# Optimization experiments

Measured on AMD Instinct MI355X. Metric: run time of the kernel, lower is better.

## Reference

```python
import jax, jax.numpy as jnp
import numpy as np

B, N, DEG, LOOKBACK, DIM, OUT = 256, 512, 16, 5, 64, 6
E = B * N * DEG            # 2,097,152 directed edges
NN = B * N                 # 131,072 nodes
K1 = int(np.ceil(0.8 * N))    # 410 nodes kept per graph after pool1
K2 = int(np.ceil(0.8 * K1))   # 328 nodes kept per graph after pool2


def setup_inputs():
    key = jax.random.key(0)
    ks = jax.random.split(key, 14)
    x = jax.random.normal(ks[0], (NN, LOOKBACK), jnp.float32)
    # per-graph random edges, then shift into the global node index space
    local = jax.random.randint(ks[1], (2, E), 0, N)
    offsets = jnp.repeat(jnp.arange(B, dtype=jnp.int32) * N, N * DEG)
    edge_index = local + offsets[None, :]

    def lin(k, fi, fo):
        return jax.random.normal(k, (fi, fo), jnp.float32) / np.sqrt(fi)

    return {
        "x": x,
        "edge_index": edge_index,
        "c1_Wl": lin(ks[2], LOOKBACK, DIM), "c1_bl": jnp.zeros((DIM,), jnp.float32),
        "c1_Wr": lin(ks[3], LOOKBACK, DIM),
        "pool1_w": jax.random.normal(ks[4], (DIM,), jnp.float32) / np.sqrt(DIM),
        "c2_Wl": lin(ks[5], DIM, DIM), "c2_bl": jnp.zeros((DIM,), jnp.float32),
        "c2_Wr": lin(ks[6], DIM, DIM),
        "pool2_w": jax.random.normal(ks[7], (DIM,), jnp.float32) / np.sqrt(DIM),
        "lin1_W": lin(ks[8], 2 * DIM, DIM), "lin1_b": jnp.zeros((DIM,), jnp.float32),
        "lin2_W": lin(ks[9], DIM, OUT), "lin2_b": jnp.zeros((OUT,), jnp.float32),
    }


def _sage(x, src, dst, valid, Wl, bl, Wr, n_nodes):
    # PyG SAGEConv: out = lin_l(mean_{j->i} x_j) + lin_r(x_i); empty nbhd -> 0
    msg = x[src] * valid[:, None]
    s = jax.ops.segment_sum(msg, dst, num_segments=n_nodes)
    deg = jax.ops.segment_sum(valid, dst, num_segments=n_nodes)
    mean = s / jnp.maximum(deg, 1.0)[:, None]
    return mean @ Wl + bl + x @ Wr


def _topk(x, w, nb, npg, k):
    # PyG TopKPooling: score = tanh(x.w/||w||), keep top-k per graph, scale kept rows
    score = jnp.tanh((x @ w) / jnp.linalg.norm(w))
    vals, idx = jax.lax.top_k(score.reshape(nb, npg), k)     # [nb, k]
    perm = (idx + (jnp.arange(nb) * npg)[:, None]).reshape(-1)
    return x[perm] * vals.reshape(-1, 1), perm


def _readout(x, nb, k):
    r = x.reshape(nb, k, -1)
    return jnp.concatenate([r.max(axis=1), r.mean(axis=1)], axis=1)  # [gmp | gap]


def reference(x, edge_index, c1_Wl, c1_bl, c1_Wr, pool1_w,
              c2_Wl, c2_bl, c2_Wr, pool2_w, lin1_W, lin1_b, lin2_W, lin2_b):
    src, dst = edge_index[0], edge_index[1]
    valid0 = jnp.ones((E,), jnp.float32)

    h = jax.nn.relu(_sage(x, src, dst, valid0, c1_Wl, c1_bl, c1_Wr, NN))
    h, perm1 = _topk(h, pool1_w, B, N, K1)
    x1 = _readout(h, B, K1)

    # filter_adj: remap edges to pooled node ids, mask dropped edges
    n1 = B * K1
    inv = jnp.full((NN,), -1, jnp.int32).at[perm1].set(jnp.arange(n1, dtype=jnp.int32))
    s1, d1 = inv[src], inv[dst]
    valid1 = ((s1 >= 0) & (d1 >= 0)).astype(jnp.float32)
    s1 = jnp.maximum(s1, 0)
    d1 = jnp.maximum(d1, 0)

    h = jax.nn.relu(_sage(h, s1, d1, valid1, c2_Wl, c2_bl, c2_Wr, n1))
    h, _ = _topk(h, pool2_w, B, K1, K2)
    x2 = _readout(h, B, K2)

    z = x1 + x2
    z = jax.nn.relu(z @ lin1_W + lin1_b)
    return z @ lin2_W + lin2_b
```

## Files before the change

### kernel.cpp

```cpp
#include <hip/hip_runtime.h>
#include <hip/hip_bf16.h>

#define BGR   256
#define NPG1  512
#define DEG   16
#define EPG   (NPG1 * DEG)
#define LB    5
#define DIM   64
#define OUTF  6
#define NN    (BGR * NPG1)
#define EDG   (BGR * EPG)
#define K1    410
#define K2    328
#define N1    (BGR * K1)
#define K1P   (K1 + 1)
#define NR    (BGR * K1P)
#define CSRW  48
#define CSRW1 52
#define GRIDW (NR / 64)
#define GRIDA (N1 / 16)

__global__ __launch_bounds__(1024)
void s1_mega_kernel(const float* __restrict__ x,
                    const int* __restrict__ eidx,
                    const float* __restrict__ Wl,
                    const float* __restrict__ bl,
                    const float* __restrict__ Wr,
                    const float* __restrict__ pw,
                    float* __restrict__ h1p,
                    float* __restrict__ x1buf,
                    unsigned short* __restrict__ csr2,
                    int* __restrict__ indeg) {
    __shared__ __align__(16) float xl[NPG1 * LB];
    __shared__ __align__(16) float ml[NPG1 * LB];
    __shared__ __align__(16) unsigned short lcsr1[CSRW1 * NPG1];
    __shared__ int   lcnt[NPG1];
    __shared__ __align__(16) float sc[NPG1];
    __shared__ int   rnk[NPG1];
    __shared__ int   rhelp[NPG1];
    __shared__ __align__(16) unsigned short lcsr2[K1 * CSRW];
    __shared__ int   lcnt2[K1];
    float* redmx = (float*)lcsr1;
    float* redsm = redmx + 16 * DIM;

    const int g = blockIdx.x, t = threadIdx.x;
    const int wid = t >> 6, lane = t & 63;
    const int n9 = t & (NPG1 - 1);
    const int half = t >> 9;
    const int* __restrict__ src = eidx;
    const int* __restrict__ dst = eidx + EDG;

    {
        const float4* x4 = (const float4*)(x + (size_t)g * (NPG1 * LB));
        float4* xl4 = (float4*)xl;
        if (t < NPG1 * LB / 4) xl4[t] = x4[t];
        if (t < NPG1) lcnt[t] = 0;
        const int fill = (K1 << 16) | K1;
        int* li = (int*)lcsr2;
        for (int i = t; i < K1 * CSRW / 2; i += 1024) li[i] = fill;
        if (t < DIM) h1p[((size_t)g * K1P + K1) * DIM + t] = 0.f;
    }
    __syncthreads();

    const int ebase = g * EPG;
    #pragma unroll
    for (int k = 0; k < EPG / 1024; ++k) {
        int e = ebase + k * 1024 + t;
        int s = src[e] & (NPG1 - 1);
        int d = dst[e] & (NPG1 - 1);
        int slot = atomicAdd(&lcnt[d], 1);
        if (slot < CSRW1) lcsr1[slot * NPG1 + d] = (unsigned short)s;
    }
    __syncthreads();

    {
        const int dgf = lcnt[n9];
        const int dg  = min(dgf, CSRW1);
        float s0 = 0.f, s1 = 0.f, s2 = 0.f, s3 = 0.f, s4 = 0.f;
        for (int k = half; k < dg; k += 2) {
            int s = lcsr1[k * NPG1 + n9];
            const float* xp = xl + s * LB;
            s0 += xp[0]; s1 += xp[1]; s2 += xp[2]; s3 += xp[3]; s4 += xp[4];
        }
        if (half == 1) {
            float* mp = ml + n9 * LB;
            mp[0] = s0; mp[1] = s1; mp[2] = s2; mp[3] = s3; mp[4] = s4;
        }
        __syncthreads();
        if (half == 0) {
            float* mp = ml + n9 * LB;
            s0 += mp[0]; s1 += mp[1]; s2 += mp[2]; s3 += mp[3]; s4 += mp[4];
            const float invd = 1.f / fmaxf((float)dgf, 1.f);
            float m[LB]  = { s0 * invd, s1 * invd, s2 * invd, s3 * invd, s4 * invd };
            float xv[LB];
            #pragma unroll
            for (int j = 0; j < LB; ++j) { xv[j] = xl[n9 * LB + j]; mp[j] = m[j]; }

            const float4* Wl4 = (const float4*)Wl;
            const float4* Wr4 = (const float4*)Wr;
            const float4* bl4 = (const float4*)bl;
            const float4* pw4 = (const float4*)pw;
            float p = 0.f, q = 0.f;
            #pragma unroll 4
            for (int d4 = 0; d4 < DIM / 4; ++d4) {
                float4 bb = bl4[d4];
                float4 ww = pw4[d4];
                float4 h = bb;
                #pragma unroll
                for (int j = 0; j < LB; ++j) {
                    float4 a = Wl4[j * (DIM / 4) + d4];
                    float4 b = Wr4[j * (DIM / 4) + d4];
                    h.x += m[j] * a.x + xv[j] * b.x;
                    h.y += m[j] * a.y + xv[j] * b.y;
                    h.z += m[j] * a.z + xv[j] * b.z;
                    h.w += m[j] * a.w + xv[j] * b.w;
                }
                h.x = fmaxf(h.x, 0.f); h.y = fmaxf(h.y, 0.f);
                h.z = fmaxf(h.z, 0.f); h.w = fmaxf(h.w, 0.f);
                p += h.x * ww.x + h.y * ww.y + h.z * ww.z + h.w * ww.w;
                q += ww.x * ww.x + ww.y * ww.y + ww.z * ww.z + ww.w * ww.w;
            }
            sc[n9] = tanhf(p / sqrtf(q));
        }
    }
    __syncthreads();

    {
        float my = sc[n9];
        int r = 0;
        const float4* sc4 = (const float4*)sc;
        const int j0 = half * (NPG1 / 8);
        #pragma unroll 4
        for (int j4 = j0; j4 < j0 + NPG1 / 8; ++j4) {
            float4 v = sc4[j4];
            int j = 4 * j4;
            r += (v.x > my) | ((v.x == my) & (j     < n9));
            r += (v.y > my) | ((v.y == my) & (j + 1 < n9));
            r += (v.z > my) | ((v.z == my) & (j + 2 < n9));
            r += (v.w > my) | ((v.w == my) & (j + 3 < n9));
        }
        if (half == 1) rhelp[n9] = r;
        __syncthreads();
        if (half == 0) rnk[n9] = r + rhelp[n9];
    }
    __syncthreads();

    if (half == 0) {
        const int rd = rnk[n9];
        if (rd < K1) {
            const int dg1 = min(lcnt[n9], CSRW1);
            int vcnt = 0;
            for (int k = 0; k < dg1; ++k) {
                int s  = lcsr1[k * NPG1 + n9];
                int rs = rnk[s];
                if (rs < K1) {
                    if (vcnt < CSRW) lcsr2[rd * CSRW + vcnt] = (unsigned short)rs;
                    ++vcnt;
                }
            }
            lcnt2[rd] = min(vcnt, CSRW);
        }
    }

    float mx = -INFINITY, sm = 0.f;
    {
        float wlv[LB], wrv[LB];
        #pragma unroll
        for (int j = 0; j < LB; ++j) { wlv[j] = Wl[j * DIM + lane]; wrv[j] = Wr[j * DIM + lane]; }
        const float blv = bl[lane];

        for (int n = wid; n < NPG1; n += 16) {
            int r = rnk[n];
            if (r >= K1) continue;
            const float* mp = ml + n * LB;
            const float* xp = xl + n * LB;
            float al = 0.f, ar = 0.f;
            #pragma unroll
            for (int j = 0; j < LB; ++j) {
                al += mp[j] * wlv[j];
                ar += xp[j] * wrv[j];
            }
            float acc = fmaxf(blv + al + ar, 0.f);
            float v = acc * sc[n];
            h1p[((size_t)g * K1P + r) * DIM + lane] = v;
            mx = fmaxf(mx, v);
            sm += v;
        }
    }
    __syncthreads();

    redmx[wid * DIM + lane] = mx;
    redsm[wid * DIM + lane] = sm;
    __syncthreads();
    if (wid == 0) {
        float m2 = redmx[lane], s2 = redsm[lane];
        #pragma unroll
        for (int w = 1; w < 16; ++w) {
            m2 = fmaxf(m2, redmx[w * DIM + lane]);
            s2 += redsm[w * DIM + lane];
        }
        x1buf[g * 2 * DIM + lane]       = m2;
        x1buf[g * 2 * DIM + DIM + lane] = s2 * (1.0f / (float)K1);
    }

    {
        const int4* ls4 = (const int4*)lcsr2;
        int4* gs4 = (int4*)(csr2 + (size_t)g * K1 * CSRW);
        for (int i = t; i < K1 * CSRW / 8; i += 1024) gs4[i] = ls4[i];
        if (t < K1) indeg[g * K1 + t] = lcnt2[t];
    }
}

__global__ __launch_bounds__(512)
void gemm2_kernel(float* __restrict__ hY,
                  float* __restrict__ Yr,
                  const float* __restrict__ Wl,
                  const float* __restrict__ bl,
                  const float* __restrict__ Wr) {
    __shared__ __align__(16) float wls[DIM * DIM];
    __shared__ __align__(16) float wrs[DIM * DIM];
    __shared__ __align__(16) float rt[64 * DIM];

    const int t = threadIdx.x, wid = t >> 6, lane = t & 63;
    const int nb = (int)blockIdx.x * 64;

    {
        const float4* W4l = (const float4*)Wl;
        const float4* W4r = (const float4*)Wr;
        const float4* R4  = (const float4*)&hY[(size_t)nb * DIM];
        float4* a = (float4*)wls;
        float4* b = (float4*)wrs;
        float4* r = (float4*)rt;
        #pragma unroll
        for (int k = 0; k < 2; ++k) {
            a[k * 512 + t] = W4l[k * 512 + t];
            b[k * 512 + t] = W4r[k * 512 + t];
            r[k * 512 + t] = R4[k * 512 + t];
        }
    }
    __syncthreads();

    const int r0 = wid * 8;
    float accl[8] = {0.f,0.f,0.f,0.f,0.f,0.f,0.f,0.f};
    float accr[8] = {0.f,0.f,0.f,0.f,0.f,0.f,0.f,0.f};
    #pragma unroll 4
    for (int j4 = 0; j4 < DIM / 4; ++j4) {
        const int jb = 4 * j4 * DIM + lane;
        float w0 = wls[jb],           w1 = wls[jb + DIM];
        float w2 = wls[jb + 2 * DIM], w3 = wls[jb + 3 * DIM];
        float u0 = wrs[jb],           u1 = wrs[jb + DIM];
        float u2 = wrs[jb + 2 * DIM], u3 = wrs[jb + 3 * DIM];
        #pragma unroll
        for (int i = 0; i < 8; ++i) {
            float4 a = *(const float4*)&rt[(r0 + i) * DIM + 4 * j4];
            accl[i] += a.x * w0 + a.y * w1 + a.z * w2 + a.w * w3;
            accr[i] += a.x * u0 + a.y * u1 + a.z * u2 + a.w * u3;
        }
    }
    const float bv = bl[lane];
    #pragma unroll
    for (int i = 0; i < 8; ++i) {
        hY[(size_t)(nb + r0 + i) * DIM + lane] = accl[i];
        Yr[(size_t)(nb + r0 + i) * DIM + lane] = accr[i] + bv;
    }
}

__global__ __launch_bounds__(256)
void gather2_kernel(const float* __restrict__ Yl,
                    float* __restrict__ Yh,
                    const unsigned short* __restrict__ csr2,
                    const int* __restrict__ indeg,
                    const float* __restrict__ pw,
                    float* __restrict__ sc2g) {
    const int t = threadIdx.x, wid = t >> 6, lane = t & 63;
    const int cid = ((int)blockIdx.x & 7) * (GRIDA / 8) + ((int)blockIdx.x >> 3);
    const int nb = __builtin_amdgcn_readfirstlane(cid * 16 + wid * 4);

    const float pwv = pw[lane];
    float q = pwv * pwv;
    #pragma unroll
    for (int o = 32; o; o >>= 1) q += __shfl_xor(q, o);
    const float inv_nrm = 1.f / sqrtf(q);

    #pragma unroll
    for (int i = 0; i < 4; ++i) {
        const int n  = nb + i;
        const int dg = indeg[n];
        const int g  = n / K1;
        const int lr = n - g * K1;
        const float* __restrict__ bp = Yl + (size_t)g * K1P * DIM;
        const int4* cr = (const int4*)(csr2 + (size_t)n * CSRW);
        float a0 = 0.f, a1 = 0.f;
        const int it = (dg + 7) >> 3;
        for (int kc = 0; kc < it; ++kc) {
            int4 wv = cr[kc];
            a0 += bp[((wv.x & 0xffff) << 6) + lane];
            a1 += bp[((wv.x >> 16)    << 6) + lane];
            a0 += bp[((wv.y & 0xffff) << 6) + lane];
            a1 += bp[((wv.y >> 16)    << 6) + lane];
            a0 += bp[((wv.z & 0xffff) << 6) + lane];
            a1 += bp[((wv.z >> 16)    << 6) + lane];
            a0 += bp[((wv.w & 0xffff) << 6) + lane];
            a1 += bp[((wv.w >> 16)    << 6) + lane];
        }
        const float invd = 1.f / fmaxf((float)dg, 1.f);
        float* yrow = Yh + (size_t)(g * K1P + lr) * DIM;
        const float h = fmaxf((a0 + a1) * invd + yrow[lane], 0.f);
        yrow[lane] = h;
        float p = h * pwv;
        #pragma unroll
        for (int o = 32; o; o >>= 1) p += __shfl_xor(p, o);
        if (lane == 0) sc2g[n] = tanhf(p * inv_nrm);
    }
}

__global__ __launch_bounds__(512)
void pool2_mlp_kernel(const float* __restrict__ sc2g,
                      const float* __restrict__ h2,
                      const float* __restrict__ x1buf,
                      const float* __restrict__ W1,
                      const float* __restrict__ b1,
                      const float* __restrict__ W2,
                      const float* __restrict__ b2,
                      float* __restrict__ out) {
    __shared__ __align__(16) float sc2[412];
    __shared__ int   rnk2[K1];
    __shared__ float redmx[8 * DIM];
    __shared__ float redsm[8 * DIM];
    __shared__ float zy[2 * DIM + DIM];

    const int g = blockIdx.x, t = threadIdx.x;
    const int wid = t >> 6, lane = t & 63;

    if (t < K1) sc2[t] = sc2g[g * K1 + t];
    if (t >= K1 && t < 412) sc2[t] = -INFINITY;
    __syncthreads();

    if (t < K1) {
        float my = sc2[t];
        int r = 0;
        const float4* sc4 = (const float4*)sc2;
        #pragma unroll 4
        for (int j4 = 0; j4 < 103; ++j4) {
            float4 v = sc4[j4];
            int j = 4 * j4;
            r += (v.x > my) | ((v.x == my) & (j     < t));
            r += (v.y > my) | ((v.y == my) & (j + 1 < t));
            r += (v.z > my) | ((v.z == my) & (j + 2 < t));
            r += (v.w > my) | ((v.w == my) & (j + 3 < t));
        }
        rnk2[t] = r;
    }
    __syncthreads();

    float mx = -INFINITY, sm = 0.f;
    for (int n = wid; n < K1; n += 8) {
        if (rnk2[n] < K2) {
            float v = h2[((size_t)g * K1P + n) * DIM + lane] * sc2[n];
            mx = fmaxf(mx, v);
            sm += v;
        }
    }
    redmx[wid * DIM + lane] = mx;
    redsm[wid * DIM + lane] = sm;
    __syncthreads();
    if (wid == 0) {
        float m2 = redmx[lane], s2 = redsm[lane];
        #pragma unroll
        for (int w = 1; w < 8; ++w) {
            m2 = fmaxf(m2, redmx[w * DIM + lane]);
            s2 += redsm[w * DIM + lane];
        }
        zy[lane]       = x1buf[g * 2 * DIM + lane]       + m2;
        zy[DIM + lane] = x1buf[g * 2 * DIM + DIM + lane] + s2 * (1.0f / (float)K2);
    }
    __syncthreads();

    if (t < DIM) {
        float a = b1[t];
        #pragma unroll 8
        for (int j = 0; j < 2 * DIM; ++j) a += zy[j] * W1[j * DIM + t];
        zy[2 * DIM + t] = fmaxf(a, 0.f);
    }
    __syncthreads();
    if (t < OUTF) {
        float a = b2[t];
        #pragma unroll
        for (int j = 0; j < DIM; ++j) a += zy[2 * DIM + j] * W2[j * OUTF + t];
        out[g * OUTF + t] = a;
    }
}

extern "C" void kernel_launch(void* const* d_in, const int* in_sizes, int n_in,
                              void* d_out, int out_size, void* d_ws, size_t ws_size,
                              hipStream_t stream) {
    (void)in_sizes; (void)n_in; (void)out_size; (void)ws_size;
    const float* x       = (const float*)d_in[0];
    const int*   eidx    = (const int*)d_in[1];
    const float* c1_Wl   = (const float*)d_in[2];
    const float* c1_bl   = (const float*)d_in[3];
    const float* c1_Wr   = (const float*)d_in[4];
    const float* pool1_w = (const float*)d_in[5];
    const float* c2_Wl   = (const float*)d_in[6];
    const float* c2_bl   = (const float*)d_in[7];
    const float* c2_Wr   = (const float*)d_in[8];
    const float* pool2_w = (const float*)d_in[9];
    const float* lin1_W  = (const float*)d_in[10];
    const float* lin1_b  = (const float*)d_in[11];
    const float* lin2_W  = (const float*)d_in[12];
    const float* lin2_b  = (const float*)d_in[13];
    float* out = (float*)d_out;

    char* w = (char*)d_ws;
    size_t off = 0;
    auto alloc = [&](size_t bytes) {
        void* p = w + off;
        off = (off + bytes + 255) & ~(size_t)255;
        return p;
    };
    float* h1p   = (float*)alloc((size_t)NR * DIM * 4);
    float* x1buf = (float*)alloc((size_t)BGR * 2 * DIM * 4);
    float* sc2g  = (float*)alloc((size_t)N1 * 4);
    int*   indeg = (int*)  alloc((size_t)N1 * 4);
    float* Yh    = (float*)alloc((size_t)NR * DIM * 4);
    unsigned short* csr2 = (unsigned short*)alloc((size_t)N1 * CSRW * 2);

    float* Yl = h1p;

    s1_mega_kernel<<<BGR, 1024, 0, stream>>>(x, eidx, c1_Wl, c1_bl, c1_Wr,
                                             pool1_w, h1p, x1buf, csr2, indeg);
    gemm2_kernel<<<GRIDW, 512, 0, stream>>>(h1p, Yh, c2_Wl, c2_bl, c2_Wr);
    gather2_kernel<<<GRIDA, 256, 0, stream>>>(Yl, Yh, csr2, indeg, pool2_w, sc2g);
    pool2_mlp_kernel<<<BGR, 512, 0, stream>>>(sc2g, Yh, x1buf, lin1_W, lin1_b,
                                              lin2_W, lin2_b, out);
}
```

Baseline: 158.6 us.

## Restructure gemm2 to per-thread row tiles with weights read via scalar loads

Rewrites the second-layer GEMM so each thread holds one full input row in registers and computes 32 output columns, with each wave handling one weight matrix and one half of the columns. Weight tiles are read straight from global memory with wave-uniform addresses, so they can use scalar or broadcast loads, which removes the shared-memory weight staging. The row tile in shared memory is XOR-swizzled to avoid bank conflicts, and the block shrinks to 256 threads. The cost is high register pressure, 64 row values plus 32 accumulators per thread, which can limit occupancy despite the launch bound. The gemm2 step is only a small part of the whole pipeline.

New measurement: 165.4 us. 1.04x slower.

```diff
diff --git a/kernel.cpp b/kernel.cpp
--- a/kernel.cpp
+++ b/kernel.cpp
@@ -211,57 +211,79 @@
     }
 }
 
-__global__ __launch_bounds__(512)
+__global__ __launch_bounds__(256, 4)
 void gemm2_kernel(float* __restrict__ hY,
                   float* __restrict__ Yr,
                   const float* __restrict__ Wl,
                   const float* __restrict__ bl,
                   const float* __restrict__ Wr) {
-    __shared__ __align__(16) float wls[DIM * DIM];
-    __shared__ __align__(16) float wrs[DIM * DIM];
     __shared__ __align__(16) float rt[64 * DIM];
 
-    const int t = threadIdx.x, wid = t >> 6, lane = t & 63;
+    const int t = threadIdx.x;
     const int nb = (int)blockIdx.x * 64;
 
     {
-        const float4* W4l = (const float4*)Wl;
-        const float4* W4r = (const float4*)Wr;
-        const float4* R4  = (const float4*)&hY[(size_t)nb * DIM];
-        float4* a = (float4*)wls;
-        float4* b = (float4*)wrs;
-        float4* r = (float4*)rt;
-        #pragma unroll
-        for (int k = 0; k < 2; ++k) {
-            a[k * 512 + t] = W4l[k * 512 + t];
-            b[k * 512 + t] = W4r[k * 512 + t];
-            r[k * 512 + t] = R4[k * 512 + t];
-        }
-    }
-    __syncthreads();
-
-    const int r0 = wid * 8;
-    float accl[8] = {0.f,0.f,0.f,0.f,0.f,0.f,0.f,0.f};
-    float accr[8] = {0.f,0.f,0.f,0.f,0.f,0.f,0.f,0.f};
-    #pragma unroll 4
-    for (int j4 = 0; j4 < DIM / 4; ++j4) {
-        const int jb = 4 * j4 * DIM + lane;
-        float w0 = wls[jb],           w1 = wls[jb + DIM];
-        float w2 = wls[jb + 2 * DIM], w3 = wls[jb + 3 * DIM];
-        float u0 = wrs[jb],           u1 = wrs[jb + DIM];
-        float u2 = wrs[jb + 2 * DIM], u3 = wrs[jb + 3 * DIM];
-        #pragma unroll
-        for (int i = 0; i < 8; ++i) {
-            float4 a = *(const float4*)&rt[(r0 + i) * DIM + 4 * j4];
-            accl[i] += a.x * w0 + a.y * w1 + a.z * w2 + a.w * w3;
-            accr[i] += a.x * u0 + a.y * u1 + a.z * u2 + a.w * u3;
-        }
-    }
-    const float bv = bl[lane];
-    #pragma unroll
-    for (int i = 0; i < 8; ++i) {
-        hY[(size_t)(nb + r0 + i) * DIM + lane] = accl[i];
-        Yr[(size_t)(nb + r0 + i) * DIM + lane] = accr[i] + bv;
+        const float4* G = (const float4*)&hY[(size_t)nb * DIM];
+        #pragma unroll
+        for (int k = 0; k < 4; ++k) {
+            int c4 = k * 256 + t;
+            int r = c4 >> 4, j4 = c4 & 15;
+            *(float4*)&rt[r * DIM + 4 * (j4 ^ (r & 15))] = G[c4];
+        }
+    }
+    __syncthreads();
+
+    const int lane = t & 63;
+    const int wid  = __builtin_amdgcn_readfirstlane(t >> 6);
+    const int cb   = (wid & 1) << 5;
+    const bool isR = (wid & 2) != 0;
+    const float* __restrict__ wmat = isR ? Wr : Wl;
+    float* __restrict__ outp = isR ? Yr : hY;
+
+    float rv[DIM];
+    #pragma unroll
+    for (int j4 = 0; j4 < 16; ++j4) {
+        float4 v = *(const float4*)&rt[lane * DIM + 4 * (j4 ^ (lane & 15))];
+        rv[4 * j4] = v.x; rv[4 * j4 + 1] = v.y;
+        rv[4 * j4 + 2] = v.z; rv[4 * j4 + 3] = v.w;
+    }
+
+    float acc[32];
+    #pragma unroll
+    for (int c = 0; c < 32; ++c) acc[c] = 0.f;
+
+    #pragma unroll
+    for (int j = 0; j < DIM; ++j) {
+        const float4* __restrict__ w4 = (const float4*)(wmat + j * DIM + cb);
+        #pragma unroll
+        for (int c4 = 0; c4 < 8; ++c4) {
+            float4 wv = w4[c4];
+            acc[4 * c4]     += rv[j] * wv.x;
+            acc[4 * c4 + 1] += rv[j] * wv.y;
+            acc[4 * c4 + 2] += rv[j] * wv.z;
+            acc[4 * c4 + 3] += rv[j] * wv.w;
+        }
+    }
+
+    if (isR) {
+        #pragma unroll
+        for (int c = 0; c < 32; ++c) acc[c] += bl[cb + c];
+    }
+
+    float* orow = outp + (size_t)(nb + lane) * DIM + cb;
+    #pragma unroll
+    for (int k = 0; k < 8; k += 4) {
+        float4 v;
+        v.x = acc[k];     v.y = acc[k + 1];
+        v.z = acc[k + 2]; v.w = acc[k + 3];
+        *(float4*)&orow[k] = v;
+    }
+    #pragma unroll
+    for (int k = 8; k < 32; k += 4) {
+        float4 v;
+        v.x = acc[k];     v.y = acc[k + 1];
+        v.z = acc[k + 2]; v.w = acc[k + 3];
+        *(float4*)&orow[k] = v;
     }
 }
 
@@ -429,7 +451,7 @@
 
     s1_mega_kernel<<<BGR, 1024, 0, stream>>>(x, eidx, c1_Wl, c1_bl, c1_Wr,
                                              pool1_w, h1p, x1buf, csr2, indeg);
-    gemm2_kernel<<<GRIDW, 512, 0, stream>>>(h1p, Yh, c2_Wl, c2_bl, c2_Wr);
+    gemm2_kernel<<<GRIDW, 256, 0, stream>>>(h1p, Yh, c2_Wl, c2_bl, c2_Wr);
     gather2_kernel<<<GRIDA, 256, 0, stream>>>(Yl, Yh, csr2, indeg, pool2_w, sc2g);
     pool2_mlp_kernel<<<BGR, 512, 0, stream>>>(sc2g, Yh, x1buf, lin1_W, lin1_b,
                                               lin2_W, lin2_b, out);
```
